# Optimization experiments

Measured on AMD Instinct MI355X. Metric: run time of the kernel, lower is better.

Reference implementation:

```python
import jax, jax.numpy as jnp
import numpy as np

B, S, IN, H, Q, M, K = 32, 2048, 128, 256, 16, 64, 3


def setup_inputs() -> dict:
    key = jax.random.key(0)
    ks = jax.random.split(key, 12)
    rn = lambda k, shp, s=0.05: (jax.random.normal(k, shp, jnp.float32) * s)
    return {
        "input_sequence": rn(ks[0], (B, S, IN), 1.0),
        "W_ih0": rn(ks[1], (4 * H, IN)),
        "W_hh0": rn(ks[2], (4 * H, H)),
        "b_ih0": jnp.zeros((4 * H,), jnp.float32),
        "b_hh0": jnp.zeros((4 * H,), jnp.float32),
        "W_ih1": rn(ks[3], (4 * H, H)),
        "W_hh1": rn(ks[4], (4 * H, H)),
        "b_ih1": jnp.zeros((4 * H,), jnp.float32),
        "b_hh1": jnp.zeros((4 * H,), jnp.float32),
        "W_cq": rn(ks[5], (Q, H)),
        "b_cq": jnp.zeros((Q,), jnp.float32),
        "mem_keys": rn(ks[6], (M, Q), 1.0),
        "mem_vals": rn(ks[7], (M, H), 1.0),
        "W_out": rn(ks[8], (H, 2 * H)),
        "b_out": jnp.zeros((H,), jnp.float32),
        "classical_weight": jnp.float32(0.7),
        "quantum_weight": jnp.float32(0.3),
    }


def _lstm_layer(x, W_ih, W_hh, b_ih, b_hh):
    """PyTorch-convention LSTM layer (gate order i,f,g,o), batch_first input."""
    Bb = x.shape[0]
    Hh = W_hh.shape[1]
    # precompute the input contribution for all timesteps: [B,S,4H]
    xg = jnp.einsum('bsi,gi->bsg', x, W_ih) + b_ih + b_hh

    def step(carry, xt):
        h, c = carry
        g = xt + h @ W_hh.T  # [B,4H]
        i, f, gg, o = jnp.split(g, 4, axis=-1)
        i = jax.nn.sigmoid(i)
        f = jax.nn.sigmoid(f)
        gg = jnp.tanh(gg)
        o = jax.nn.sigmoid(o)
        c = f * c + i * gg
        h = o * jnp.tanh(c)
        return (h, c), h

    init = (jnp.zeros((Bb, Hh), x.dtype), jnp.zeros((Bb, Hh), x.dtype))
    _, hs = jax.lax.scan(step, init, jnp.swapaxes(xg, 0, 1))  # [S,B,H]
    return jnp.swapaxes(hs, 0, 1)


def _forward(input_sequence, W_ih0, W_hh0, b_ih0, b_hh0, W_ih1, W_hh1, b_ih1,
             b_hh1, W_cq, b_cq, mem_keys, mem_vals, W_out, b_out,
             classical_weight, quantum_weight):
    # classical 2-layer LSTM
    h1 = _lstm_layer(input_sequence, W_ih0, W_hh0, b_ih0, b_hh0)
    lstm_out = _lstm_layer(h1, W_ih1, W_hh1, b_ih1, b_hh1)  # [B,S,H]

    # classical_to_quantum + tanh -> per-token query [B,S,Q]
    q = jnp.tanh(jnp.einsum('bsh,qh->bsq', lstm_out, W_cq) + b_cq)

    # batched k-NN read over the quantum memory (cosine similarity, k=3)
    eps = jnp.float32(1e-8)
    qn = q / (jnp.linalg.norm(q, axis=-1, keepdims=True) + eps)
    kn = mem_keys / (jnp.linalg.norm(mem_keys, axis=-1, keepdims=True) + eps)
    sims = jnp.einsum('bsq,mq->bsm', qn, kn)          # [B,S,M]
    top_vals, top_idx = jax.lax.top_k(sims, K)        # [B,S,K]
    gathered = mem_vals[top_idx]                      # [B,S,K,H]

    # similarity-weighted average of retrieved contents
    tot = jnp.sum(top_vals, axis=-1, keepdims=True)   # [B,S,1]
    weighted = jnp.einsum('bsk,bskh->bsh', top_vals, gathered)
    enhanced = jnp.where(tot > 0, weighted / jnp.where(tot == 0, 1.0, tot), 0.0)

    # combine streams and project
    combined = jnp.concatenate(
        [classical_weight * lstm_out, quantum_weight * enhanced], axis=-1)
    out = jnp.einsum('bsc,hc->bsh', combined, W_out) + b_out  # [B,S,H]
    return out


def reference(input_sequence, W_ih0, W_hh0, b_ih0, b_hh0, W_ih1, W_hh1, b_ih1,
              b_hh1, W_cq, b_cq, mem_keys, mem_vals, W_out, b_out,
              classical_weight, quantum_weight):
    return _forward(input_sequence, W_ih0, W_hh0, b_ih0, b_hh0, W_ih1, W_hh1,
                    b_ih1, b_hh1, W_cq, b_cq, mem_keys, mem_vals, W_out, b_out,
                    classical_weight, quantum_weight)
```

## Files before the change

kernel.cpp:

```cpp
#include <hip/hip_runtime.h>
#include <cstdint>
#include <cstddef>
#include <math.h>

#define B_   32
#define S_   2048
#define IN_  128
#define H_   256
#define Q_   16
#define M_   64
#define D_   4

typedef unsigned long long u64;
typedef __attribute__((ext_vector_type(2))) unsigned int u32x2;

__device__ __forceinline__ float4 ld4(const float* p) { return *(const float4*)p; }

#define AGLD64(p)    __hip_atomic_load((p),  __ATOMIC_RELAXED, __HIP_MEMORY_SCOPE_AGENT)
#define AGST64(p, v) __hip_atomic_store((p), (v), __ATOMIC_RELAXED, __HIP_MEMORY_SCOPE_AGENT)

__device__ __forceinline__ u32x2 mall_load_u64(const u64* p) {
  u32x2 q;
  asm volatile("global_load_dwordx2 %0, %1, off sc0 sc1\n\ts_waitcnt vmcnt(0)"
               : "=v"(q) : "v"(p) : "memory");
  return q;
}
__device__ __forceinline__ void mall_issue1(const u64* p, u32x2& q) {
  asm volatile("global_load_dwordx2 %0, %1, off sc0 sc1"
               : "=&v"(q) : "v"(p) : "memory");
}
__device__ __forceinline__ void mall_wait1(u32x2& q) {
  asm volatile("s_waitcnt vmcnt(0)" : "+v"(q) :: "memory");
}

__device__ __forceinline__ float sigm_f(float x) { return 1.0f / (1.0f + __expf(-x)); }
__device__ __forceinline__ float tanh_f(float x) { return 1.0f - 2.0f / (__expf(2.0f * x) + 1.0f); }

__global__ __launch_bounds__(512, 1) void lstm2(
    const float* __restrict__ x,
    const float* __restrict__ Wih0, const float* __restrict__ bih0,
    const float* __restrict__ bhh0, const float* __restrict__ Whh0,
    const float* __restrict__ Wih1, const float* __restrict__ bih1,
    const float* __restrict__ bhh1, const float* __restrict__ Whh1,
    float* __restrict__ out,
    u64* __restrict__ exs)
{
  const int f = blockIdx.x;
  const int n = f & 7;
  const int b = f >> 3;

  const int tid = threadIdx.x;
  const int w   = tid >> 6;
  const int l   = tid & 63;
  const int kc  = l & 15;
  const int rg  = l >> 4;
  const int wrg = w * 4 + rg;
  const int col = n * 32 + wrg;

  __shared__ float w1[128][257];
  __shared__ float aring[4][256];
  __shared__ float hring[2][256];
  __shared__ float x_sh[2][IN_];

  for (int i = tid; i < 4 * 256; i += 512) ((float*)aring)[i] = 0.0f;
  for (int i = tid; i < 2 * 256; i += 512) ((float*)hring)[i] = 0.0f;

  float4 wf0[4][4], wf1[4][4], wi0[4][2];
  float rb0[4], rb1[4];
#pragma unroll
  for (int g = 0; g < 4; g++) {
    const int row = g * 256 + col;
    const float* p0 = Whh0 + (size_t)row * 256 + 4 * kc;
    const float* p1 = Whh1 + (size_t)row * 256 + 4 * kc;
    const float* pi = Wih0 + (size_t)row * 128 + 4 * kc;
#pragma unroll
    for (int j = 0; j < 4; j++) {
      wf0[g][j] = ld4(p0 + 64 * j);
      wf1[g][j] = ld4(p1 + 64 * j);
    }
#pragma unroll
    for (int j = 0; j < 2; j++) wi0[g][j] = ld4(pi + 64 * j);
    rb0[g] = bih0[row] + bhh0[row];
    rb1[g] = bih1[row] + bhh1[row];
    const float* pw = Wih1 + (size_t)row * 256 + 4 * kc;
    float* dst = &w1[g * 32 + wrg][4 * kc];
#pragma unroll
    for (int j = 0; j < 4; j++) *(float4*)(dst + 64 * j) = ld4(pw + 64 * j);
  }

  const float* xrow = x + (size_t)b * S_ * IN_;
  float* outp = out + (size_t)b * S_ * H_;
  u64* exb = exs + (size_t)b * 1024;

  if (tid < IN_) {
    x_sh[0][tid] = xrow[tid];
    x_sh[1][tid] = xrow[IN_ + tid];
  }
  float xreg = (tid < IN_) ? xrow[(size_t)2 * IN_ + tid] : 0.0f;
  float cst0 = 0.0f, cst1 = 0.0f;
  float xa0s[4], xa1s[4] = {0, 0, 0, 0};
  __syncthreads();

  {
    const float* xb = x_sh[0];
    float4 xv[2];
#pragma unroll
    for (int j = 0; j < 2; j++) xv[j] = ld4(xb + 4 * kc + 64 * j);
#pragma unroll
    for (int g = 0; g < 4; g++) {
      float4 s4 = {0, 0, 0, 0};
#pragma unroll
      for (int j = 0; j < 2; j++) {
        s4.x += wi0[g][j].x * xv[j].x; s4.y += wi0[g][j].y * xv[j].y;
        s4.z += wi0[g][j].z * xv[j].z; s4.w += wi0[g][j].w * xv[j].w;
      }
      float s = (s4.x + s4.y) + (s4.z + s4.w);
      s += __shfl_xor(s, 1); s += __shfl_xor(s, 2);
      s += __shfl_xor(s, 4); s += __shfl_xor(s, 8);
      xa0s[g] = s + rb0[g];
    }
  }

  bool dead = false;
  for (int t = 0; t < S_ + D_; ++t) {
    const bool doA = (t < S_);
    const int  u   = t - D_;
    const bool doH = (u >= 0);
    const int  pa = t & 1, ph = u & 1;
    const unsigned eA = (unsigned)(t + 1), eH = (unsigned)(u + 1);

    float xreg_n = 0.0f;
    if (tid < IN_ && t + 2 < S_) {
      int tn = (t + 3 < S_) ? t + 3 : S_ - 1;
      xreg_n = xrow[(size_t)tn * IN_ + tid];
    }

    if (doA) {
      const float* ap = aring[(t - 1) & 3];
      float4 av[4];
#pragma unroll
      for (int j = 0; j < 4; j++) av[j] = ld4(ap + 4 * kc + 64 * j);
      float gv[4];
#pragma unroll
      for (int g = 0; g < 4; g++) {
        float4 s4 = {0, 0, 0, 0};
#pragma unroll
        for (int j = 0; j < 4; j++) {
          s4.x += wf0[g][j].x * av[j].x; s4.y += wf0[g][j].y * av[j].y;
          s4.z += wf0[g][j].z * av[j].z; s4.w += wf0[g][j].w * av[j].w;
        }
        float s = (s4.x + s4.y) + (s4.z + s4.w);
        s += __shfl_xor(s, 1); s += __shfl_xor(s, 2);
        s += __shfl_xor(s, 4); s += __shfl_xor(s, 8);
        gv[g] = s + xa0s[g];
      }
      float ig = sigm_f(gv[0]), fg = sigm_f(gv[1]);
      float cg = tanh_f(gv[2]), og = sigm_f(gv[3]);
      cst0 = fg * cst0 + ig * cg;
      float a = og * tanh_f(cst0);
      if (kc == 0) {
        u64 pk = ((u64)eA << 32) | (u64)__float_as_uint(a);
        AGST64(exb + (pa << 8) + col, pk);
        aring[t & 3][col] = a;
      }
    }
    if (doH) {
      const float* hp = hring[(u - 1) & 1];
      float4 hv[4];
#pragma unroll
      for (int j = 0; j < 4; j++) hv[j] = ld4(hp + 4 * kc + 64 * j);
      float gv[4];
#pragma unroll
      for (int g = 0; g < 4; g++) {
        float4 s4 = {0, 0, 0, 0};
#pragma unroll
        for (int j = 0; j < 4; j++) {
          s4.x += wf1[g][j].x * hv[j].x; s4.y += wf1[g][j].y * hv[j].y;
          s4.z += wf1[g][j].z * hv[j].z; s4.w += wf1[g][j].w * hv[j].w;
        }
        float s = (s4.x + s4.y) + (s4.z + s4.w);
        s += __shfl_xor(s, 1); s += __shfl_xor(s, 2);
        s += __shfl_xor(s, 4); s += __shfl_xor(s, 8);
        gv[g] = s + xa1s[g];
      }
      float ig = sigm_f(gv[0]), fg = sigm_f(gv[1]);
      float cg = tanh_f(gv[2]), og = sigm_f(gv[3]);
      cst1 = fg * cst1 + ig * cg;
      float h = og * tanh_f(cst1);
      if (kc == 0) {
        u64 pk = ((u64)eH << 32) | (u64)__float_as_uint(h);
        AGST64(exb + ((2 + ph) << 8) + col, pk);
        outp[(size_t)u * H_ + col] = h;
        hring[u & 1][col] = h;
      }
    }

    const bool isA = (tid < 256);
    const int  e   = tid & 255;
    const bool ownp = ((e >> 5) == n);
    const bool act  = isA ? doA : doH;
    const bool need = act && !ownp && !dead;
    const unsigned etag = isA ? eA : eH;
    const int plane = isA ? pa : 2 + ph;
    u64* bp = exb + (plane << 8) + e;
    u32x2 q;
    if (need) mall_issue1(bp, q);

    if (t + 1 < S_) {
      const float* xb = x_sh[(t + 1) & 1];
      float4 xv[2];
#pragma unroll
      for (int j = 0; j < 2; j++) xv[j] = ld4(xb + 4 * kc + 64 * j);
#pragma unroll
      for (int g = 0; g < 4; g++) {
        float4 s4 = {0, 0, 0, 0};
#pragma unroll
        for (int j = 0; j < 2; j++) {
          s4.x += wi0[g][j].x * xv[j].x; s4.y += wi0[g][j].y * xv[j].y;
          s4.z += wi0[g][j].z * xv[j].z; s4.w += wi0[g][j].w * xv[j].w;
        }
        float s = (s4.x + s4.y) + (s4.z + s4.w);
        s += __shfl_xor(s, 1); s += __shfl_xor(s, 2);
        s += __shfl_xor(s, 4); s += __shfl_xor(s, 8);
        xa0s[g] = s + rb0[g];
      }
    }
    {
      const int v = t - D_ + 1;
      if (v >= 0 && v < S_) {
        const float* avp = aring[v & 3];
        float4 av[4];
#pragma unroll
        for (int j = 0; j < 4; j++) av[j] = ld4(avp + 4 * kc + 64 * j);
#pragma unroll
        for (int g = 0; g < 4; g++) {
          const float* wr = &w1[g * 32 + wrg][4 * kc];
          float4 s4 = {0, 0, 0, 0};
#pragma unroll
          for (int j = 0; j < 4; j++) {
            float4 wv = ld4(wr + 64 * j);
            s4.x += wv.x * av[j].x; s4.y += wv.y * av[j].y;
            s4.z += wv.z * av[j].z; s4.w += wv.w * av[j].w;
          }
          float s = (s4.x + s4.y) + (s4.z + s4.w);
          s += __shfl_xor(s, 1); s += __shfl_xor(s, 2);
          s += __shfl_xor(s, 4); s += __shfl_xor(s, 8);
          xa1s[g] = s + rb1[g];
        }
      }
    }

    if (need) {
      mall_wait1(q);
      bool got = (q.y == etag);
#pragma unroll 1
      for (int it = 0; it < 16 && !got; ++it) {
        q = mall_load_u64(bp);
        got = (q.y == etag);
      }
      if (!got) {
        unsigned guard = 0;
        while (!got) {
          u64 v2 = AGLD64(bp);
          if ((unsigned)(v2 >> 32) == etag) { q.x = (unsigned)v2; got = true; }
          if (++guard >= (1u << 20)) { dead = true; break; }
        }
      }
      if (isA) aring[t & 3][e] = __uint_as_float(q.x);
      else     hring[u & 1][e] = __uint_as_float(q.x);
    }

    if (tid < IN_ && t < S_) x_sh[t & 1][tid] = xreg;
    xreg = xreg_n;
    __syncthreads();
  }
}

__global__ __launch_bounds__(256) void knn_enh(
    const float* __restrict__ lstm, const float* __restrict__ Wcq,
    const float* __restrict__ bcq, const float* __restrict__ keys,
    const float* __restrict__ vals, const float* __restrict__ qwp,
    float* __restrict__ enh)
{
  const int tid  = threadIdx.x;
  const int wave = tid >> 6, lane = tid & 63;
  const int t = blockIdx.x * 4 + wave;

  __shared__ float xsh[4][256];
  __shared__ float qsh[4][16];

  const float* xrow = lstm + (size_t)t * H_;
  float4 x4 = ld4(xrow + lane * 4);
  *(float4*)&xsh[wave][lane * 4] = x4;
  __syncthreads();

  const int j = lane & 15, seg = lane >> 4;
  const float* wrow = Wcq + j * H_ + seg * 64;
  const float* xseg = &xsh[wave][seg * 64];
  float p = 0.0f;
#pragma unroll
  for (int c = 0; c < 64; c += 4) {
    float4 w4 = ld4(wrow + c);
    p += w4.x * xseg[c] + w4.y * xseg[c + 1] + w4.z * xseg[c + 2] + w4.w * xseg[c + 3];
  }
  p += __shfl_xor(p, 16);
  p += __shfl_xor(p, 32);
  float q = tanhf(p + bcq[j]);

  float sq = q * q;
  sq += __shfl_xor(sq, 1); sq += __shfl_xor(sq, 2);
  sq += __shfl_xor(sq, 4); sq += __shfl_xor(sq, 8);
  float qn = q / (sqrtf(sq) + 1e-8f);
  if (lane < 16) qsh[wave][lane] = qn;
  __syncthreads();

  const int m = lane;
  const float* krow = keys + m * Q_;
  float kv[16]; float kn2 = 0.0f;
#pragma unroll
  for (int jj = 0; jj < 16; jj++) { kv[jj] = krow[jj]; kn2 += kv[jj] * kv[jj]; }
  float rn = 1.0f / (sqrtf(kn2) + 1e-8f);
  float sim = 0.0f;
#pragma unroll
  for (int jj = 0; jj < 16; jj++) sim += qsh[wave][jj] * kv[jj];
  sim *= rn;

  float rem = sim;
  float tv[3]; int ti[3];
#pragma unroll
  for (int k = 0; k < 3; k++) {
    float v = rem; int idx = m;
#pragma unroll
    for (int d = 1; d < 64; d <<= 1) {
      float ov = __shfl_xor(v, d);
      int   oi = __shfl_xor(idx, d);
      if (ov > v || (ov == v && oi < idx)) { v = ov; idx = oi; }
    }
    tv[k] = v; ti[k] = idx;
    if (m == idx) rem = -INFINITY;
  }
  float tot = tv[0] + tv[1] + tv[2];

  float ex = 0, ey = 0, ez = 0, ew = 0;
#pragma unroll
  for (int k = 0; k < 3; k++) {
    float4 vv = ld4(vals + (size_t)ti[k] * H_ + lane * 4);
    ex += tv[k] * vv.x; ey += tv[k] * vv.y;
    ez += tv[k] * vv.z; ew += tv[k] * vv.w;
  }
  float inv = (tot > 0.0f) ? 1.0f / tot : 0.0f;
  const float qw = qwp[0];

  float4 o;
  o.x = qw * ex * inv; o.y = qw * ey * inv;
  o.z = qw * ez * inv; o.w = qw * ew * inv;
  *(float4*)&enh[(size_t)t * H_ + lane * 4] = o;
}

__global__ __launch_bounds__(256) void gemm_cat(
    float* __restrict__ io, const float* __restrict__ A2,
    const float* __restrict__ Bw, const float* __restrict__ bias,
    const float* __restrict__ cwp)
{
  __shared__ float As[16][68];
  __shared__ float Bs[16][260];
  const int tid  = threadIdx.x;
  const int row0 = blockIdx.x * 64;
  const int tx = tid & 15, ty = tid >> 4;
  const int lr = tid >> 2;
  const int lk = (tid & 3) << 2;
  const float cw = cwp[0];

  float acc[4][16];
#pragma unroll
  for (int i = 0; i < 4; i++)
#pragma unroll
    for (int j = 0; j < 16; j++) acc[i][j] = 0.0f;

  for (int k0 = 0; k0 < 512; k0 += 16) {
    float4 av;
    if (k0 < 256) {
      av = ld4(io + (size_t)(row0 + lr) * 256 + k0 + lk);
      av.x *= cw; av.y *= cw; av.z *= cw; av.w *= cw;
    } else {
      av = ld4(A2 + (size_t)(row0 + lr) * 256 + (k0 - 256) + lk);
    }
    As[lk + 0][lr] = av.x; As[lk + 1][lr] = av.y;
    As[lk + 2][lr] = av.z; As[lk + 3][lr] = av.w;
    const float* bp = Bw + (size_t)tid * 512 + k0;
#pragma unroll
    for (int q = 0; q < 4; q++) {
      float4 b4 = ld4(bp + 4 * q);
      Bs[4 * q + 0][tid] = b4.x; Bs[4 * q + 1][tid] = b4.y;
      Bs[4 * q + 2][tid] = b4.z; Bs[4 * q + 3][tid] = b4.w;
    }
    __syncthreads();
#pragma unroll
    for (int k = 0; k < 16; k++) {
      float4 a4 = *(const float4*)&As[k][ty << 2];
      float aa[4] = {a4.x, a4.y, a4.z, a4.w};
#pragma unroll
      for (int cc = 0; cc < 4; cc++) {
        float4 b4 = *(const float4*)&Bs[k][cc * 64 + (tx << 2)];
        float bb[4] = {b4.x, b4.y, b4.z, b4.w};
#pragma unroll
        for (int i = 0; i < 4; i++)
#pragma unroll
          for (int jj = 0; jj < 4; jj++) acc[i][cc * 4 + jj] += aa[i] * bb[jj];
      }
    }
    __syncthreads();
  }

#pragma unroll
  for (int i = 0; i < 4; i++) {
#pragma unroll
    for (int cc = 0; cc < 4; cc++) {
      int c0 = cc * 64 + (tx << 2);
      float4 o;
      o.x = acc[i][cc * 4 + 0] + bias[c0 + 0];
      o.y = acc[i][cc * 4 + 1] + bias[c0 + 1];
      o.z = acc[i][cc * 4 + 2] + bias[c0 + 2];
      o.w = acc[i][cc * 4 + 3] + bias[c0 + 3];
      *(float4*)&io[(size_t)(row0 + (ty << 2) + i) * 256 + c0] = o;
    }
  }
}

extern "C" void kernel_launch(void* const* d_in, const int* in_sizes, int n_in,
                              void* d_out, int out_size, void* d_ws, size_t ws_size,
                              hipStream_t stream)
{
  const float* x    = (const float*)d_in[0];
  const float* Wih0 = (const float*)d_in[1];
  const float* Whh0 = (const float*)d_in[2];
  const float* bih0 = (const float*)d_in[3];
  const float* bhh0 = (const float*)d_in[4];
  const float* Wih1 = (const float*)d_in[5];
  const float* Whh1 = (const float*)d_in[6];
  const float* bih1 = (const float*)d_in[7];
  const float* bhh1 = (const float*)d_in[8];
  const float* Wcq  = (const float*)d_in[9];
  const float* bcq  = (const float*)d_in[10];
  const float* keys = (const float*)d_in[11];
  const float* vals = (const float*)d_in[12];
  const float* Wout = (const float*)d_in[13];
  const float* bout = (const float*)d_in[14];
  const float* cw   = (const float*)d_in[15];
  const float* qw   = (const float*)d_in[16];
  float* out = (float*)d_out;

  const size_t HE = (size_t)B_ * S_ * H_;
  if (ws_size < HE * sizeof(float)) return;
  u64* exs = (u64*)d_ws;
  float* enh = (float*)d_ws;

  const int MT = B_ * S_;

  hipMemsetAsync(exs, 0, (size_t)32 * 1024 * sizeof(u64), stream);
  lstm2<<<dim3(256), dim3(512), 0, stream>>>(x, Wih0, bih0, bhh0, Whh0,
                                             Wih1, bih1, bhh1, Whh1, out, exs);

  knn_enh<<<dim3(MT / 4), dim3(256), 0, stream>>>(out, Wcq, bcq, keys, vals, qw, enh);

  gemm_cat<<<dim3(MT / 64), dim3(256), 0, stream>>>(out, enh, Wout, bout, cw);
}
```

Measured before the change: 13.05 ms.

## Split each batch's LSTM across 16 smaller blocks with wider pipelined exchange polling

Each batch's two-layer LSTM is now spread over 16 workgroups of 256 threads (16 hidden columns each) instead of 8 workgroups of 512, which doubles the grid and halves the Wih1 shared-memory tile. The cross-block exchange now has each thread poll two adjacent tagged entries with one 16-byte load, keeping two loads in flight and using a wave-wide exit check. Own-block values are no longer written locally and are read back through the exchange buffer. The output store and next-x prefetch move after the exchange. The aim is more parallelism and fewer, wider polling loads, at the cost of more blocks in the global handshake and more exchange traffic per step.

```diff
diff --git a/kernel.cpp b/kernel.cpp
--- a/kernel.cpp
+++ b/kernel.cpp
@@ -12,31 +12,17 @@
 #define D_   4
 
 typedef unsigned long long u64;
-typedef __attribute__((ext_vector_type(2))) unsigned int u32x2;
+typedef __attribute__((ext_vector_type(4))) unsigned int u32x4;
 
 __device__ __forceinline__ float4 ld4(const float* p) { return *(const float4*)p; }
 
 #define AGLD64(p)    __hip_atomic_load((p),  __ATOMIC_RELAXED, __HIP_MEMORY_SCOPE_AGENT)
 #define AGST64(p, v) __hip_atomic_store((p), (v), __ATOMIC_RELAXED, __HIP_MEMORY_SCOPE_AGENT)
 
-__device__ __forceinline__ u32x2 mall_load_u64(const u64* p) {
-  u32x2 q;
-  asm volatile("global_load_dwordx2 %0, %1, off sc0 sc1\n\ts_waitcnt vmcnt(0)"
-               : "=v"(q) : "v"(p) : "memory");
-  return q;
-}
-__device__ __forceinline__ void mall_issue1(const u64* p, u32x2& q) {
-  asm volatile("global_load_dwordx2 %0, %1, off sc0 sc1"
-               : "=&v"(q) : "v"(p) : "memory");
-}
-__device__ __forceinline__ void mall_wait1(u32x2& q) {
-  asm volatile("s_waitcnt vmcnt(0)" : "+v"(q) :: "memory");
-}
-
 __device__ __forceinline__ float sigm_f(float x) { return 1.0f / (1.0f + __expf(-x)); }
 __device__ __forceinline__ float tanh_f(float x) { return 1.0f - 2.0f / (__expf(2.0f * x) + 1.0f); }
 
-__global__ __launch_bounds__(512, 1) void lstm2(
+__global__ __launch_bounds__(256, 2) void lstm2(
     const float* __restrict__ x,
     const float* __restrict__ Wih0, const float* __restrict__ bih0,
     const float* __restrict__ bhh0, const float* __restrict__ Whh0,
@@ -46,8 +32,8 @@
     u64* __restrict__ exs)
 {
   const int f = blockIdx.x;
-  const int n = f & 7;
-  const int b = f >> 3;
+  const int n = f & 15;
+  const int b = f >> 4;
 
   const int tid = threadIdx.x;
   const int w   = tid >> 6;
@@ -55,15 +41,15 @@
   const int kc  = l & 15;
   const int rg  = l >> 4;
   const int wrg = w * 4 + rg;
-  const int col = n * 32 + wrg;
-
-  __shared__ float w1[128][257];
+  const int col = n * 16 + wrg;
+
+  __shared__ float w1[64][257];
   __shared__ float aring[4][256];
   __shared__ float hring[2][256];
   __shared__ float x_sh[2][IN_];
 
-  for (int i = tid; i < 4 * 256; i += 512) ((float*)aring)[i] = 0.0f;
-  for (int i = tid; i < 2 * 256; i += 512) ((float*)hring)[i] = 0.0f;
+  for (int i = tid; i < 4 * 256; i += 256) ((float*)aring)[i] = 0.0f;
+  for (int i = tid; i < 2 * 256; i += 256) ((float*)hring)[i] = 0.0f;
 
   float4 wf0[4][4], wf1[4][4], wi0[4][2];
   float rb0[4], rb1[4];
@@ -83,7 +69,7 @@
     rb0[g] = bih0[row] + bhh0[row];
     rb1[g] = bih1[row] + bhh1[row];
     const float* pw = Wih1 + (size_t)row * 256 + 4 * kc;
-    float* dst = &w1[g * 32 + wrg][4 * kc];
+    float* dst = &w1[g * 16 + wrg][4 * kc];
 #pragma unroll
     for (int j = 0; j < 4; j++) *(float4*)(dst + 64 * j) = ld4(pw + 64 * j);
   }
@@ -121,6 +107,8 @@
     }
   }
 
+  const bool isA = (tid < 128);
+  const int  pi  = tid & 127;
   bool dead = false;
   for (int t = 0; t < S_ + D_; ++t) {
     const bool doA = (t < S_);
@@ -129,12 +117,6 @@
     const int  pa = t & 1, ph = u & 1;
     const unsigned eA = (unsigned)(t + 1), eH = (unsigned)(u + 1);
 
-    float xreg_n = 0.0f;
-    if (tid < IN_ && t + 2 < S_) {
-      int tn = (t + 3 < S_) ? t + 3 : S_ - 1;
-      xreg_n = xrow[(size_t)tn * IN_ + tid];
-    }
-
     if (doA) {
       const float* ap = aring[(t - 1) & 3];
       float4 av[4];
@@ -161,9 +143,9 @@
       if (kc == 0) {
         u64 pk = ((u64)eA << 32) | (u64)__float_as_uint(a);
         AGST64(exb + (pa << 8) + col, pk);
-        aring[t & 3][col] = a;
-      }
-    }
+      }
+    }
+    float hval = 0.0f;
     if (doH) {
       const float* hp = hring[(u - 1) & 1];
       float4 hv[4];
@@ -186,25 +168,12 @@
       float ig = sigm_f(gv[0]), fg = sigm_f(gv[1]);
       float cg = tanh_f(gv[2]), og = sigm_f(gv[3]);
       cst1 = fg * cst1 + ig * cg;
-      float h = og * tanh_f(cst1);
+      hval = og * tanh_f(cst1);
       if (kc == 0) {
-        u64 pk = ((u64)eH << 32) | (u64)__float_as_uint(h);
+        u64 pk = ((u64)eH << 32) | (u64)__float_as_uint(hval);
         AGST64(exb + ((2 + ph) << 8) + col, pk);
-        outp[(size_t)u * H_ + col] = h;
-        hring[u & 1][col] = h;
-      }
-    }
-
-    const bool isA = (tid < 256);
-    const int  e   = tid & 255;
-    const bool ownp = ((e >> 5) == n);
-    const bool act  = isA ? doA : doH;
-    const bool need = act && !ownp && !dead;
-    const unsigned etag = isA ? eA : eH;
-    const int plane = isA ? pa : 2 + ph;
-    u64* bp = exb + (plane << 8) + e;
-    u32x2 q;
-    if (need) mall_issue1(bp, q);
+      }
+    }
 
     if (t + 1 < S_) {
       const float* xb = x_sh[(t + 1) & 1];
@@ -234,7 +203,7 @@
         for (int j = 0; j < 4; j++) av[j] = ld4(avp + 4 * kc + 64 * j);
 #pragma unroll
         for (int g = 0; g < 4; g++) {
-          const float* wr = &w1[g * 32 + wrg][4 * kc];
+          const float* wr = &w1[g * 16 + wrg][4 * kc];
           float4 s4 = {0, 0, 0, 0};
 #pragma unroll
           for (int j = 0; j < 4; j++) {
@@ -250,28 +219,55 @@
       }
     }
 
-    if (need) {
-      mall_wait1(q);
-      bool got = (q.y == etag);
+    {
+      const bool active = isA ? doA : doH;
+      if (active && !dead) {
+        u64* bp = exb + ((isA ? pa : (2 + ph)) << 8) + 2 * pi;
+        const unsigned et = isA ? eA : eH;
+        unsigned v0 = 0, v1 = 0;
+        bool got = false;
+        u32x4 q0, q1;
+        asm volatile("s_waitcnt vmcnt(0)" ::: "memory");
+        asm volatile("global_load_dwordx4 %0, %1, off sc0 sc1"
+                     : "=&v"(q0) : "v"(bp) : "memory");
 #pragma unroll 1
-      for (int it = 0; it < 16 && !got; ++it) {
-        q = mall_load_u64(bp);
-        got = (q.y == etag);
-      }
-      if (!got) {
-        unsigned guard = 0;
-        while (!got) {
-          u64 v2 = AGLD64(bp);
-          if ((unsigned)(v2 >> 32) == etag) { q.x = (unsigned)v2; got = true; }
-          if (++guard >= (1u << 20)) { dead = true; break; }
-        }
-      }
-      if (isA) aring[t & 3][e] = __uint_as_float(q.x);
-      else     hring[u & 1][e] = __uint_as_float(q.x);
-    }
-
+        for (int it = 0; it < 12; ++it) {
+          asm volatile("global_load_dwordx4 %0, %1, off sc0 sc1"
+                       : "=&v"(q1) : "v"(bp) : "memory");
+          asm volatile("s_waitcnt vmcnt(1)" : "+v"(q0) :: "memory");
+          if (!got && q0.y == et && q0.w == et) { v0 = q0.x; v1 = q0.z; got = true; }
+          if (__all(got)) { asm volatile("s_waitcnt vmcnt(0)" : "+v"(q1) :: "memory"); break; }
+          asm volatile("global_load_dwordx4 %0, %1, off sc0 sc1"
+                       : "=&v"(q0) : "v"(bp) : "memory");
+          asm volatile("s_waitcnt vmcnt(1)" : "+v"(q1) :: "memory");
+          if (!got && q1.y == et && q1.w == et) { v0 = q1.x; v1 = q1.z; got = true; }
+          if (__all(got)) { asm volatile("s_waitcnt vmcnt(0)" : "+v"(q0) :: "memory"); break; }
+        }
+        if (!__all(got)) asm volatile("s_waitcnt vmcnt(0)" ::: "memory");
+        if (!got) {
+          unsigned guard = 0; bool g0 = false, g1 = false;
+          while (!(g0 && g1)) {
+            if (!g0) { u64 w0 = AGLD64(bp);     if ((unsigned)(w0 >> 32) == et) { v0 = (unsigned)w0; g0 = true; } }
+            if (!g1) { u64 w1 = AGLD64(bp + 1); if ((unsigned)(w1 >> 32) == et) { v1 = (unsigned)w1; g1 = true; } }
+            if (++guard >= (1u << 20)) { dead = true; break; }
+          }
+        }
+        if (isA) {
+          aring[t & 3][2 * pi]     = __uint_as_float(v0);
+          aring[t & 3][2 * pi + 1] = __uint_as_float(v1);
+        } else {
+          hring[u & 1][2 * pi]     = __uint_as_float(v0);
+          hring[u & 1][2 * pi + 1] = __uint_as_float(v1);
+        }
+      }
+    }
+
+    if (doH && kc == 0) outp[(size_t)u * H_ + col] = hval;
     if (tid < IN_ && t < S_) x_sh[t & 1][tid] = xreg;
-    xreg = xreg_n;
+    if (tid < IN_ && t + 2 < S_) {
+      int tn = (t + 3 < S_) ? t + 3 : S_ - 1;
+      xreg = xrow[(size_t)tn * IN_ + tid];
+    }
     __syncthreads();
   }
 }
@@ -458,7 +454,7 @@
   const int MT = B_ * S_;
 
   hipMemsetAsync(exs, 0, (size_t)32 * 1024 * sizeof(u64), stream);
-  lstm2<<<dim3(256), dim3(512), 0, stream>>>(x, Wih0, bih0, bhh0, Whh0,
+  lstm2<<<dim3(512), dim3(256), 0, stream>>>(x, Wih0, bih0, bhh0, Whh0,
                                              Wih1, bih1, bhh1, Whh1, out, exs);
 
   knn_enh<<<dim3(MT / 4), dim3(256), 0, stream>>>(out, Wcq, bcq, keys, vals, qw, enh);
```

Measured after the change: 12.89 ms. About the same (-1.2%).
